# Kernel tuning notes

Hardware: AMD Instinct MI355X
Metric: run time of the kernel (lower is better)

## Reference

```python
import jax, jax.numpy as jnp
import numpy as np

MODEL_DIM = 512
HEAD_NUM = 8
HEAD_DIM = 64
INNER_DIM = HEAD_NUM * HEAD_DIM  # 512
B, L, S = 4, 2048, 2048


def setup_inputs() -> dict:
    key = jax.random.key(0)
    ks = jax.random.split(key, 7)
    query = jax.random.normal(ks[0], (B, L, MODEL_DIM), dtype=jnp.float32)
    key_t = jax.random.normal(ks[1], (B, S, MODEL_DIM), dtype=jnp.float32)
    value = jax.random.normal(ks[2], (B, S, MODEL_DIM), dtype=jnp.float32)
    # nn.Linear weights stored as [out, in]; applied as x @ W.T
    sc = 1.0 / np.sqrt(MODEL_DIM)
    Wq = jax.random.uniform(ks[3], (INNER_DIM, MODEL_DIM), jnp.float32, -sc, sc)
    Wk = jax.random.uniform(ks[4], (INNER_DIM, MODEL_DIM), jnp.float32, -sc, sc)
    Wv = jax.random.uniform(ks[5], (INNER_DIM, MODEL_DIM), jnp.float32, -sc, sc)
    Wo = jax.random.uniform(ks[6], (MODEL_DIM, INNER_DIM), jnp.float32, -sc, sc)
    return {"query": query, "key": key_t, "value": value,
            "Wq": Wq, "Wk": Wk, "Wv": Wv, "Wo": Wo}


def reference(query, key, value, Wq, Wk, Wv, Wo):
    temperature = HEAD_DIM ** 0.5
    # projections: [b, n, inner]
    q = query @ Wq.T
    k = key @ Wk.T
    v = value @ Wv.T
    # split heads: b n (h d) -> b n h d
    q = q.reshape(B, L, HEAD_NUM, HEAD_DIM)
    k = k.reshape(B, S, HEAD_NUM, HEAD_DIM)
    v = v.reshape(B, S, HEAD_NUM, HEAD_DIM)
    # full attention (FullAttention): scores [b, l, s, h]
    qk = jnp.einsum('blhd,bshd->blsh', q / temperature, k)
    z = jax.nn.softmax(qk, axis=2)
    attended = jnp.einsum('blsh,bshd->blhd', z, v)
    # merge heads: b l h d -> b l (h d), then output projection
    attended = attended.reshape(B, L, INNER_DIM)
    return attended @ Wo.T
```

## Files before the change

kernel.cpp:

```cpp
#include <hip/hip_runtime.h>
#include <stdint.h>
#include <stddef.h>

#define NB 4
#define NL 2048
#define MODEL 512
#define NH 8
#define HD 64

#define QSCALE 0.18033688011112042f

typedef __attribute__((ext_vector_type(8))) short short8;
typedef __attribute__((ext_vector_type(8))) __bf16 bf16x8;
typedef __attribute__((ext_vector_type(4))) float f32x4;
typedef __attribute__((ext_vector_type(16))) float f32x16;
typedef __attribute__((ext_vector_type(2))) unsigned int u32x2;

static __device__ __forceinline__ unsigned short f2bf(float x) {
  union { float f; unsigned u; } v; v.f = x;
  unsigned r = v.u + 0x7FFFu + ((v.u >> 16) & 1u);
  return (unsigned short)(r >> 16);
}

static __device__ __forceinline__ unsigned cvtpk(float lo, float hi) {
  unsigned r;
  asm("v_cvt_pk_bf16_f32 %0, %1, %2" : "=v"(r) : "v"(lo), "v"(hi));
  return r;
}

static __device__ __forceinline__ f32x4 mfma16(short8 a, short8 b, f32x4 c) {
  return __builtin_amdgcn_mfma_f32_16x16x32_bf16(
      __builtin_bit_cast(bf16x8, a), __builtin_bit_cast(bf16x8, b), c, 0, 0, 0);
}

static __device__ __forceinline__ f32x16 mfma32(short8 a, short8 b, f32x16 c) {
  return __builtin_amdgcn_mfma_f32_32x32x16_bf16(
      __builtin_bit_cast(bf16x8, a), __builtin_bit_cast(bf16x8, b), c, 0, 0, 0);
}

#define GLOAD_LDS(gp, lp)                                                      \
  __builtin_amdgcn_global_load_lds(                                            \
      (const __attribute__((address_space(1))) void*)(gp),                     \
      (__attribute__((address_space(3))) void*)(lp), 16, 0, 0)

__global__ __launch_bounds__(256) void qkv512(const float* __restrict__ Aq,
                                              const float* __restrict__ Ak,
                                              const float* __restrict__ Av,
                                              const float* __restrict__ Wqp,
                                              const float* __restrict__ Wkp,
                                              const float* __restrict__ Wvp,
                                              unsigned short* __restrict__ Qo,
                                              unsigned short* __restrict__ Ko,
                                              unsigned short* __restrict__ Vto) {
  __shared__ unsigned short Alds[128][72];
  __shared__ unsigned short Wlds[128][72];

  const int which = blockIdx.x >> 8;
  const int bid = blockIdx.x & 255;
  const float* A = which == 0 ? Aq : which == 1 ? Ak : Av;
  const float* W = which == 0 ? Wqp : which == 1 ? Wkp : Wvp;

  const int tid = threadIdx.x;
  const int bn = bid & 3;
  const int bm = bid >> 2;
  const int mbase = bm * 128, nbase = bn * 128;
  const int wid = tid >> 6, lane = tid & 63;
  const int lo = lane & 15, grp = lane >> 4;
  const int wm = wid >> 1, wn = wid & 1;

  f32x4 acc[4][4] = {};

#pragma unroll 1
  for (int kb = 0; kb < 8; ++kb) {
#pragma unroll
    for (int it = 0; it < 8; ++it) {
      int id = tid + it * 256;
      int row = id >> 4, cg = id & 15;
      float4 v = *(const float4*)(A + (size_t)(mbase + row) * 512 + kb * 64 + cg * 4);
      uint2 w; w.x = cvtpk(v.x, v.y); w.y = cvtpk(v.z, v.w);
      *(uint2*)&Alds[row][cg * 4] = w;
    }
#pragma unroll
    for (int it = 0; it < 8; ++it) {
      int id = tid + it * 256;
      int row = id >> 4, cg = id & 15;
      float4 v = *(const float4*)(W + (size_t)(nbase + row) * 512 + kb * 64 + cg * 4);
      uint2 w; w.x = cvtpk(v.x, v.y); w.y = cvtpk(v.z, v.w);
      *(uint2*)&Wlds[row][cg * 4] = w;
    }
    __syncthreads();

#pragma unroll
    for (int kk = 0; kk < 2; ++kk) {
      short8 aw[4], ba[4];
#pragma unroll
      for (int f = 0; f < 4; ++f)
        aw[f] = *(const short8*)&Wlds[wn * 64 + f * 16 + lo][kk * 32 + grp * 8];
#pragma unroll
      for (int f = 0; f < 4; ++f)
        ba[f] = *(const short8*)&Alds[wm * 64 + f * 16 + lo][kk * 32 + grp * 8];
#pragma unroll
      for (int mf = 0; mf < 4; ++mf)
#pragma unroll
        for (int nf = 0; nf < 4; ++nf)
          acc[mf][nf] = mfma16(aw[nf], ba[mf], acc[mf][nf]);
    }
    __syncthreads();
  }

  const float scale = (which == 0) ? QSCALE : 1.0f;
#pragma unroll
  for (int mf = 0; mf < 4; ++mf)
#pragma unroll
    for (int nf = 0; nf < 4; ++nf) {
      int m = mbase + wm * 64 + mf * 16 + lo;
      int n0 = nbase + wn * 64 + nf * 16 + grp * 4;
      f32x4 a = acc[mf][nf];
      if (which < 2) {
        unsigned short* C = which == 0 ? Qo : Ko;
        uint2 w;
        w.x = cvtpk(a[0] * scale, a[1] * scale);
        w.y = cvtpk(a[2] * scale, a[3] * scale);
        *(uint2*)(C + (size_t)m * 512 + n0) = w;
      } else {
        int b = m >> 11, s = m & 2047;
#pragma unroll
        for (int i = 0; i < 4; ++i)
          Vto[((size_t)b * 512 + n0 + i) * 2048 + s] = f2bf(a[i]);
      }
    }
}

__global__ __launch_bounds__(512) void gemmWo(const unsigned short* __restrict__ A,
                                              const float* __restrict__ W,
                                              float* __restrict__ C) {
  __shared__ unsigned short Alds[128][72];
  __shared__ unsigned short Wlds[128][72];

  const int tid = threadIdx.x;
  const int bn = blockIdx.x & 3;
  const int bm = blockIdx.x >> 2;
  const int mbase = bm * 128, nbase = bn * 128;
  const int wid = tid >> 6, lane = tid & 63;
  const int lo = lane & 15, grp = lane >> 4;
  const int wm = wid >> 2, wn = wid & 3;

  f32x4 acc[4][2] = {};

#pragma unroll 1
  for (int kb = 0; kb < 8; ++kb) {
#pragma unroll
    for (int it = 0; it < 2; ++it) {
      int id = tid + it * 512;
      int row = id >> 3, cg = id & 7;
      uint4 v = *(const uint4*)(A + (size_t)(mbase + row) * 512 + kb * 64 + cg * 8);
      *(uint4*)&Alds[row][cg * 8] = v;
    }
#pragma unroll
    for (int it = 0; it < 4; ++it) {
      int id = tid + it * 512;
      int row = id >> 4, cg = id & 15;
      float4 v = *(const float4*)(W + (size_t)(nbase + row) * 512 + kb * 64 + cg * 4);
      uint2 w; w.x = cvtpk(v.x, v.y); w.y = cvtpk(v.z, v.w);
      *(uint2*)&Wlds[row][cg * 4] = w;
    }
    __syncthreads();

#pragma unroll
    for (int kk = 0; kk < 2; ++kk) {
      short8 aw[2], ba[4];
#pragma unroll
      for (int f = 0; f < 2; ++f)
        aw[f] = *(const short8*)&Wlds[wn * 32 + f * 16 + lo][kk * 32 + grp * 8];
#pragma unroll
      for (int f = 0; f < 4; ++f)
        ba[f] = *(const short8*)&Alds[wm * 64 + f * 16 + lo][kk * 32 + grp * 8];
#pragma unroll
      for (int mf = 0; mf < 4; ++mf)
#pragma unroll
        for (int nf = 0; nf < 2; ++nf)
          acc[mf][nf] = mfma16(aw[nf], ba[mf], acc[mf][nf]);
    }
    __syncthreads();
  }

#pragma unroll
  for (int mf = 0; mf < 4; ++mf)
#pragma unroll
    for (int nf = 0; nf < 2; ++nf) {
      int m = mbase + wm * 64 + mf * 16 + lo;
      int n0 = nbase + wn * 32 + nf * 16 + grp * 4;
      f32x4 a = acc[mf][nf];
      float4 o;
      o.x = a[0]; o.y = a[1]; o.z = a[2]; o.w = a[3];
      *(float4*)(C + (size_t)m * 512 + n0) = o;
    }
}

__global__ __launch_bounds__(256, 2) void attn64(const unsigned short* __restrict__ Qg,
                                                 const unsigned short* __restrict__ Kg,
                                                 const unsigned short* __restrict__ Vt,
                                                 unsigned short* __restrict__ Og) {
  __shared__ __align__(16) char LDS[65536];
  char* Kbase = LDS;
  char* Vbase = LDS + 32768;
  float* cb = (float*)LDS;

  const int tid = threadIdx.x;
  const int wid = tid >> 6, lane = tid & 63;
  const int ln31 = lane & 31, hl = lane >> 5;
  const int qh = wid & 1, sh = wid >> 1;

  const int lb = ((blockIdx.x & 7) << 6) | (blockIdx.x >> 3);
  const int bh = lb >> 4, qb = lb & 15;
  const int b = bh >> 3, h = bh & 7;

  const unsigned short* Kbh = Kg + (size_t)b * 2048 * 512 + h * 64;
  const unsigned short* Vbh = Vt + ((size_t)b * 512 + h * 64) * 2048;

  const int q0 = qb * 128 + qh * 64 + ln31;

  short8 qfA[4], qfB[4];
#pragma unroll
  for (int ks = 0; ks < 4; ++ks) {
    qfA[ks] = *(const short8*)(Qg + ((size_t)b * 2048 + q0) * 512 + h * 64 + ks * 16 + hl * 8);
    qfB[ks] = *(const short8*)(Qg + ((size_t)b * 2048 + q0 + 32) * 512 + h * 64 + ks * 16 + hl * 8);
  }

  const int srow = lane >> 3;
  const int schunk = (lane & 7) ^ srow;
  const unsigned short* kgp = Kbh + (size_t)(sh * 16 * 64 + qh * 32 + srow) * 512 + schunk * 8;
  const unsigned short* vgp = Vbh + (size_t)(qh * 32 + srow) * 2048 + sh * 16 * 64 + schunk * 8;
  char* kd = Kbase + sh * 16384;
  char* vd = Vbase + sh * 16384;
  const int wofs = qh * 4096;

  const int rb0 = ln31 * 128, rb1 = rb0 + 4096;
  const int sw = (ln31 & 7) << 4;
  const int hl16 = hl * 16;

  const short8 ones = {0x3F80, 0x3F80, 0x3F80, 0x3F80, 0x3F80, 0x3F80, 0x3F80, 0x3F80};
  f32x16 oA0 = {}, oA1 = {}, oB0 = {}, oB1 = {}, lA = {}, lB = {};

#pragma unroll
  for (int g = 0; g < 4; ++g) {
    GLOAD_LDS(kgp + (size_t)g * 8 * 512, kd + wofs + g * 1024);
    GLOAD_LDS(vgp + (size_t)g * 8 * 2048, vd + wofs + g * 1024);
  }
  __syncthreads();

  int cur = 0;
#pragma unroll 1
  for (int t = 0; t < 16; ++t) {
    if (t < 15) {
      const unsigned short* kp = kgp + (size_t)(t + 1) * 64 * 512;
      const unsigned short* vp = vgp + (t + 1) * 64;
      char* kdn = kd + (cur ^ 1) * 8192 + wofs;
      char* vdn = vd + (cur ^ 1) * 8192 + wofs;
#pragma unroll
      for (int g = 0; g < 4; ++g) {
        GLOAD_LDS(kp + (size_t)g * 8 * 512, kdn + g * 1024);
        GLOAD_LDS(vp + (size_t)g * 8 * 2048, vdn + g * 1024);
      }
    }

    const char* kr = kd + cur * 8192;
    const char* vr = vd + cur * 8192;

    f32x16 sA0 = {}, sB0 = {};
#pragma unroll
    for (int ks = 0; ks < 4; ++ks) {
      short8 k0 = *(const short8*)(kr + rb0 + ((ks * 32 + hl16) ^ sw));
      sA0 = mfma32(k0, qfA[ks], sA0);
      sB0 = mfma32(k0, qfB[ks], sB0);
    }
    f32x16 sA1 = {}, sB1 = {};
#pragma unroll
    for (int ks = 0; ks < 4; ++ks) {
      short8 k1 = *(const short8*)(kr + rb1 + ((ks * 32 + hl16) ^ sw));
      sA1 = mfma32(k1, qfA[ks], sA1);
      sB1 = mfma32(k1, qfB[ks], sB1);
    }

    unsigned cA0[8], cB0[8];
#pragma unroll
    for (int i = 0; i < 8; ++i)
      cA0[i] = cvtpk(__builtin_exp2f(sA0[2 * i]), __builtin_exp2f(sA0[2 * i + 1]));
#pragma unroll
    for (int i = 0; i < 8; ++i)
      cB0[i] = cvtpk(__builtin_exp2f(sB0[2 * i]), __builtin_exp2f(sB0[2 * i + 1]));
    {
      u32x2 r;
      r = __builtin_amdgcn_permlane32_swap(cA0[0], cA0[2], false, false); cA0[0] = r[0]; cA0[2] = r[1];
      r = __builtin_amdgcn_permlane32_swap(cA0[1], cA0[3], false, false); cA0[1] = r[0]; cA0[3] = r[1];
      r = __builtin_amdgcn_permlane32_swap(cA0[4], cA0[6], false, false); cA0[4] = r[0]; cA0[6] = r[1];
      r = __builtin_amdgcn_permlane32_swap(cA0[5], cA0[7], false, false); cA0[5] = r[0]; cA0[7] = r[1];
      r = __builtin_amdgcn_permlane32_swap(cB0[0], cB0[2], false, false); cB0[0] = r[0]; cB0[2] = r[1];
      r = __builtin_amdgcn_permlane32_swap(cB0[1], cB0[3], false, false); cB0[1] = r[0]; cB0[3] = r[1];
      r = __builtin_amdgcn_permlane32_swap(cB0[4], cB0[6], false, false); cB0[4] = r[0]; cB0[6] = r[1];
      r = __builtin_amdgcn_permlane32_swap(cB0[5], cB0[7], false, false); cB0[5] = r[0]; cB0[7] = r[1];
    }
    short8 pfA0, pfA1, pfB0, pfB1;
    {
      union { unsigned u[4]; short8 s; } t2;
      t2.u[0] = cA0[0]; t2.u[1] = cA0[1]; t2.u[2] = cA0[2]; t2.u[3] = cA0[3]; pfA0 = t2.s;
      t2.u[0] = cA0[4]; t2.u[1] = cA0[5]; t2.u[2] = cA0[6]; t2.u[3] = cA0[7]; pfA1 = t2.s;
      t2.u[0] = cB0[0]; t2.u[1] = cB0[1]; t2.u[2] = cB0[2]; t2.u[3] = cB0[3]; pfB0 = t2.s;
      t2.u[0] = cB0[4]; t2.u[1] = cB0[5]; t2.u[2] = cB0[6]; t2.u[3] = cB0[7]; pfB1 = t2.s;
    }

#pragma unroll
    for (int ks = 0; ks < 2; ++ks) {
      short8 pf = ks ? pfA1 : pfA0;
      short8 pg = ks ? pfB1 : pfB0;
      short8 v0 = *(const short8*)(vr + rb0 + ((ks * 32 + hl16) ^ sw));
      short8 v1 = *(const short8*)(vr + rb1 + ((ks * 32 + hl16) ^ sw));
      oA0 = mfma32(v0, pf, oA0);
      oA1 = mfma32(v1, pf, oA1);
      oB0 = mfma32(v0, pg, oB0);
      oB1 = mfma32(v1, pg, oB1);
      lA = mfma32(ones, pf, lA);
      lB = mfma32(ones, pg, lB);
    }

    unsigned cA1[8], cB1[8];
#pragma unroll
    for (int i = 0; i < 8; ++i)
      cA1[i] = cvtpk(__builtin_exp2f(sA1[2 * i]), __builtin_exp2f(sA1[2 * i + 1]));
#pragma unroll
    for (int i = 0; i < 8; ++i)
      cB1[i] = cvtpk(__builtin_exp2f(sB1[2 * i]), __builtin_exp2f(sB1[2 * i + 1]));
    {
      u32x2 r;
      r = __builtin_amdgcn_permlane32_swap(cA1[0], cA1[2], false, false); cA1[0] = r[0]; cA1[2] = r[1];
      r = __builtin_amdgcn_permlane32_swap(cA1[1], cA1[3], false, false); cA1[1] = r[0]; cA1[3] = r[1];
      r = __builtin_amdgcn_permlane32_swap(cA1[4], cA1[6], false, false); cA1[4] = r[0]; cA1[6] = r[1];
      r = __builtin_amdgcn_permlane32_swap(cA1[5], cA1[7], false, false); cA1[5] = r[0]; cA1[7] = r[1];
      r = __builtin_amdgcn_permlane32_swap(cB1[0], cB1[2], false, false); cB1[0] = r[0]; cB1[2] = r[1];
      r = __builtin_amdgcn_permlane32_swap(cB1[1], cB1[3], false, false); cB1[1] = r[0]; cB1[3] = r[1];
      r = __builtin_amdgcn_permlane32_swap(cB1[4], cB1[6], false, false); cB1[4] = r[0]; cB1[6] = r[1];
      r = __builtin_amdgcn_permlane32_swap(cB1[5], cB1[7], false, false); cB1[5] = r[0]; cB1[7] = r[1];
    }
    short8 pfA2, pfA3, pfB2, pfB3;
    {
      union { unsigned u[4]; short8 s; } t2;
      t2.u[0] = cA1[0]; t2.u[1] = cA1[1]; t2.u[2] = cA1[2]; t2.u[3] = cA1[3]; pfA2 = t2.s;
      t2.u[0] = cA1[4]; t2.u[1] = cA1[5]; t2.u[2] = cA1[6]; t2.u[3] = cA1[7]; pfA3 = t2.s;
      t2.u[0] = cB1[0]; t2.u[1] = cB1[1]; t2.u[2] = cB1[2]; t2.u[3] = cB1[3]; pfB2 = t2.s;
      t2.u[0] = cB1[4]; t2.u[1] = cB1[5]; t2.u[2] = cB1[6]; t2.u[3] = cB1[7]; pfB3 = t2.s;
    }

#pragma unroll
    for (int ks = 2; ks < 4; ++ks) {
      short8 pf = (ks == 2) ? pfA2 : pfA3;
      short8 pg = (ks == 2) ? pfB2 : pfB3;
      short8 v0 = *(const short8*)(vr + rb0 + ((ks * 32 + hl16) ^ sw));
      short8 v1 = *(const short8*)(vr + rb1 + ((ks * 32 + hl16) ^ sw));
      oA0 = mfma32(v0, pf, oA0);
      oA1 = mfma32(v1, pf, oA1);
      oB0 = mfma32(v0, pg, oB0);
      oB1 = mfma32(v1, pg, oB1);
      lA = mfma32(ones, pf, lA);
      lB = mfma32(ones, pg, lB);
    }

    __syncthreads();
    cur ^= 1;
  }

  float* myc = cb + (size_t)(qh * 64 + lane) * 68;
  if (sh == 1) {
    float4* c4 = (float4*)myc;
#pragma unroll
    for (int i = 0; i < 4; ++i) {
      c4[i]      = make_float4(oA0[4*i], oA0[4*i+1], oA0[4*i+2], oA0[4*i+3]);
      c4[4 + i]  = make_float4(oA1[4*i], oA1[4*i+1], oA1[4*i+2], oA1[4*i+3]);
      c4[8 + i]  = make_float4(oB0[4*i], oB0[4*i+1], oB0[4*i+2], oB0[4*i+3]);
      c4[12 + i] = make_float4(oB1[4*i], oB1[4*i+1], oB1[4*i+2], oB1[4*i+3]);
    }
    myc[64] = lA[0]; myc[65] = lB[0];
  }
  __syncthreads();
  if (sh == 0) {
#pragma unroll
    for (int i = 0; i < 16; ++i) {
      oA0[i] += myc[i];      oA1[i] += myc[16 + i];
      oB0[i] += myc[32 + i]; oB1[i] += myc[48 + i];
    }
    float invA = 1.f / (lA[0] + myc[64]);
    float invB = 1.f / (lB[0] + myc[65]);

#pragma unroll
    for (int dblk = 0; dblk < 2; ++dblk) {
      const f32x16& a = dblk ? oA1 : oA0;
      const f32x16& bb = dblk ? oB1 : oB0;
#pragma unroll
      for (int rg = 0; rg < 4; ++rg) {
        int d0 = dblk * 32 + rg * 8 + hl * 4;
        uint2 w;
        w.x = cvtpk(a[rg * 4 + 0] * invA, a[rg * 4 + 1] * invA);
        w.y = cvtpk(a[rg * 4 + 2] * invA, a[rg * 4 + 3] * invA);
        *(uint2*)(Og + ((size_t)b * 2048 + q0) * 512 + h * 64 + d0) = w;
        w.x = cvtpk(bb[rg * 4 + 0] * invB, bb[rg * 4 + 1] * invB);
        w.y = cvtpk(bb[rg * 4 + 2] * invB, bb[rg * 4 + 3] * invB);
        *(uint2*)(Og + ((size_t)b * 2048 + q0 + 32) * 512 + h * 64 + d0) = w;
      }
    }
  }
}

extern "C" void kernel_launch(void* const* d_in, const int* in_sizes, int n_in,
                              void* d_out, int out_size, void* d_ws, size_t ws_size,
                              hipStream_t stream) {
  (void)in_sizes; (void)n_in; (void)out_size; (void)ws_size;
  const float* query = (const float*)d_in[0];
  const float* key   = (const float*)d_in[1];
  const float* value = (const float*)d_in[2];
  const float* Wq    = (const float*)d_in[3];
  const float* Wk    = (const float*)d_in[4];
  const float* Wv    = (const float*)d_in[5];
  const float* Wo    = (const float*)d_in[6];

  const size_t TOK = (size_t)NB * NL * MODEL;
  unsigned short* Qw = (unsigned short*)d_ws;
  unsigned short* Kw = Qw + TOK;
  unsigned short* Vw = Kw + TOK;
  unsigned short* Aw = Vw + TOK;

  qkv512<<<768, 256, 0, stream>>>(query, key, value, Wq, Wk, Wv, Qw, Kw, Vw);
  attn64<<<512, 256, 0, stream>>>(Qw, Kw, Vw, Aw);
  gemmWo<<<256, 512, 0, stream>>>(Aw, Wo, (float*)d_out);
}
```

Before: 115.1 us.

## Register-prefetch next K tile in QKV and Wo projection GEMMs

Both projection GEMMs now load the next K-slice from global memory into registers before running the MFMA loop on the current LDS tile. After a barrier, they convert and store that slice to LDS, so global latency overlaps compute. The QKV kernel also gets an occupancy hint of 3 blocks per SM via launch_bounds. The cost is more registers held across the loop, plus an extra barrier per iteration.

```diff
diff --git a/kernel.cpp b/kernel.cpp
--- a/kernel.cpp
+++ b/kernel.cpp
@@ -43,15 +43,15 @@
       (const __attribute__((address_space(1))) void*)(gp),                     \
       (__attribute__((address_space(3))) void*)(lp), 16, 0, 0)
 
-__global__ __launch_bounds__(256) void qkv512(const float* __restrict__ Aq,
-                                              const float* __restrict__ Ak,
-                                              const float* __restrict__ Av,
-                                              const float* __restrict__ Wqp,
-                                              const float* __restrict__ Wkp,
-                                              const float* __restrict__ Wvp,
-                                              unsigned short* __restrict__ Qo,
-                                              unsigned short* __restrict__ Ko,
-                                              unsigned short* __restrict__ Vto) {
+__global__ __launch_bounds__(256, 3) void qkv512(const float* __restrict__ Aq,
+                                                 const float* __restrict__ Ak,
+                                                 const float* __restrict__ Av,
+                                                 const float* __restrict__ Wqp,
+                                                 const float* __restrict__ Wkp,
+                                                 const float* __restrict__ Wvp,
+                                                 unsigned short* __restrict__ Qo,
+                                                 unsigned short* __restrict__ Ko,
+                                                 unsigned short* __restrict__ Vto) {
   __shared__ unsigned short Alds[128][72];
   __shared__ unsigned short Wlds[128][72];
 
@@ -68,27 +68,39 @@
   const int lo = lane & 15, grp = lane >> 4;
   const int wm = wid >> 1, wn = wid & 1;
 
+  const float* Arow[8];
+  const float* Wrow[8];
+#pragma unroll
+  for (int it = 0; it < 8; ++it) {
+    int id = tid + it * 256, row = id >> 4, cg = id & 15;
+    Arow[it] = A + (size_t)(mbase + row) * 512 + cg * 4;
+    Wrow[it] = W + (size_t)(nbase + row) * 512 + cg * 4;
+  }
+
   f32x4 acc[4][4] = {};
+  float4 ra[8], rw[8];
+
+#pragma unroll
+  for (int it = 0; it < 8; ++it) { ra[it] = *(const float4*)Arow[it]; rw[it] = *(const float4*)Wrow[it]; }
+#pragma unroll
+  for (int it = 0; it < 8; ++it) {
+    int id = tid + it * 256, row = id >> 4, cg = id & 15;
+    uint2 wa; wa.x = cvtpk(ra[it].x, ra[it].y); wa.y = cvtpk(ra[it].z, ra[it].w);
+    *(uint2*)&Alds[row][cg * 4] = wa;
+    uint2 ww; ww.x = cvtpk(rw[it].x, rw[it].y); ww.y = cvtpk(rw[it].z, rw[it].w);
+    *(uint2*)&Wlds[row][cg * 4] = ww;
+  }
+  __syncthreads();
 
 #pragma unroll 1
   for (int kb = 0; kb < 8; ++kb) {
-#pragma unroll
-    for (int it = 0; it < 8; ++it) {
-      int id = tid + it * 256;
-      int row = id >> 4, cg = id & 15;
-      float4 v = *(const float4*)(A + (size_t)(mbase + row) * 512 + kb * 64 + cg * 4);
-      uint2 w; w.x = cvtpk(v.x, v.y); w.y = cvtpk(v.z, v.w);
-      *(uint2*)&Alds[row][cg * 4] = w;
-    }
-#pragma unroll
-    for (int it = 0; it < 8; ++it) {
-      int id = tid + it * 256;
-      int row = id >> 4, cg = id & 15;
-      float4 v = *(const float4*)(W + (size_t)(nbase + row) * 512 + kb * 64 + cg * 4);
-      uint2 w; w.x = cvtpk(v.x, v.y); w.y = cvtpk(v.z, v.w);
-      *(uint2*)&Wlds[row][cg * 4] = w;
-    }
-    __syncthreads();
+    if (kb < 7) {
+#pragma unroll
+      for (int it = 0; it < 8; ++it) {
+        ra[it] = *(const float4*)(Arow[it] + (kb + 1) * 64);
+        rw[it] = *(const float4*)(Wrow[it] + (kb + 1) * 64);
+      }
+    }
 
 #pragma unroll
     for (int kk = 0; kk < 2; ++kk) {
@@ -106,6 +118,18 @@
           acc[mf][nf] = mfma16(aw[nf], ba[mf], acc[mf][nf]);
     }
     __syncthreads();
+
+    if (kb < 7) {
+#pragma unroll
+      for (int it = 0; it < 8; ++it) {
+        int id = tid + it * 256, row = id >> 4, cg = id & 15;
+        uint2 wa; wa.x = cvtpk(ra[it].x, ra[it].y); wa.y = cvtpk(ra[it].z, ra[it].w);
+        *(uint2*)&Alds[row][cg * 4] = wa;
+        uint2 ww; ww.x = cvtpk(rw[it].x, rw[it].y); ww.y = cvtpk(rw[it].z, rw[it].w);
+        *(uint2*)&Wlds[row][cg * 4] = ww;
+      }
+      __syncthreads();
+    }
   }
 
   const float scale = (which == 0) ? QSCALE : 1.0f;
@@ -145,26 +169,47 @@
   const int lo = lane & 15, grp = lane >> 4;
   const int wm = wid >> 2, wn = wid & 3;
 
+  const unsigned short* Asrc[2];
+  const float* Wsrc[4];
+#pragma unroll
+  for (int it = 0; it < 2; ++it) {
+    int id = tid + it * 512, row = id >> 3, cg = id & 7;
+    Asrc[it] = A + (size_t)(mbase + row) * 512 + cg * 8;
+  }
+#pragma unroll
+  for (int it = 0; it < 4; ++it) {
+    int id = tid + it * 512, row = id >> 4, cg = id & 15;
+    Wsrc[it] = W + (size_t)(nbase + row) * 512 + cg * 4;
+  }
+
   f32x4 acc[4][2] = {};
+  uint4 rA[2]; float4 rW[4];
+
+#pragma unroll
+  for (int it = 0; it < 2; ++it) rA[it] = *(const uint4*)Asrc[it];
+#pragma unroll
+  for (int it = 0; it < 4; ++it) rW[it] = *(const float4*)Wsrc[it];
+#pragma unroll
+  for (int it = 0; it < 2; ++it) {
+    int id = tid + it * 512, row = id >> 3, cg = id & 7;
+    *(uint4*)&Alds[row][cg * 8] = rA[it];
+  }
+#pragma unroll
+  for (int it = 0; it < 4; ++it) {
+    int id = tid + it * 512, row = id >> 4, cg = id & 15;
+    uint2 w; w.x = cvtpk(rW[it].x, rW[it].y); w.y = cvtpk(rW[it].z, rW[it].w);
+    *(uint2*)&Wlds[row][cg * 4] = w;
+  }
+  __syncthreads();
 
 #pragma unroll 1
   for (int kb = 0; kb < 8; ++kb) {
-#pragma unroll
-    for (int it = 0; it < 2; ++it) {
-      int id = tid + it * 512;
-      int row = id >> 3, cg = id & 7;
-      uint4 v = *(const uint4*)(A + (size_t)(mbase + row) * 512 + kb * 64 + cg * 8);
-      *(uint4*)&Alds[row][cg * 8] = v;
-    }
-#pragma unroll
-    for (int it = 0; it < 4; ++it) {
-      int id = tid + it * 512;
-      int row = id >> 4, cg = id & 15;
-      float4 v = *(const float4*)(W + (size_t)(nbase + row) * 512 + kb * 64 + cg * 4);
-      uint2 w; w.x = cvtpk(v.x, v.y); w.y = cvtpk(v.z, v.w);
-      *(uint2*)&Wlds[row][cg * 4] = w;
-    }
-    __syncthreads();
+    if (kb < 7) {
+#pragma unroll
+      for (int it = 0; it < 2; ++it) rA[it] = *(const uint4*)(Asrc[it] + (kb + 1) * 64);
+#pragma unroll
+      for (int it = 0; it < 4; ++it) rW[it] = *(const float4*)(Wsrc[it] + (kb + 1) * 64);
+    }
 
 #pragma unroll
     for (int kk = 0; kk < 2; ++kk) {
@@ -182,6 +227,21 @@
           acc[mf][nf] = mfma16(aw[nf], ba[mf], acc[mf][nf]);
     }
     __syncthreads();
+
+    if (kb < 7) {
+#pragma unroll
+      for (int it = 0; it < 2; ++it) {
+        int id = tid + it * 512, row = id >> 3, cg = id & 7;
+        *(uint4*)&Alds[row][cg * 8] = rA[it];
+      }
+#pragma unroll
+      for (int it = 0; it < 4; ++it) {
+        int id = tid + it * 512, row = id >> 4, cg = id & 15;
+        uint2 w; w.x = cvtpk(rW[it].x, rW[it].y); w.y = cvtpk(rW[it].z, rW[it].w);
+        *(uint2*)&Wlds[row][cg * 4] = w;
+      }
+      __syncthreads();
+    }
   }
 
 #pragma unroll
```

Result: slower. 145.5 us (+26.4%).
